# Kernel tuning notes

Measured on AMD Instinct MI355X. Metric: run time of the kernel, lower is better.

Reference implementation:

```python
import jax, jax.numpy as jnp
import numpy as np

B, N, NT, ET = 16, 38, 9, 4
NE = N * (N - 1) // 2          # 703 edge-generation steps
R = N + NE                     # repeat_num = 741 masked subgraphs
H = D = 128                    # nhid / nout
L = 12                         # num_flow_layer
EDIM = ET - 1                  # 3 relation types used by RGCN
EPS = 1e-5
TEMP = 0.1                     # straight-through argmax temperature


def _st_dis(x, w1, b1, w2, b2):
    # MLP -> logits -> straight-through one-hot(argmax)
    h = jnp.tanh(x @ w1.T + b1)
    logits = h @ w2.T + b2
    soft = jax.nn.softmax(logits / TEMP, axis=-1)
    hard = jax.nn.one_hot(jnp.argmax(logits, axis=-1), logits.shape[-1], dtype=logits.dtype)
    return soft + jax.lax.stop_gradient(hard - soft)


def _one_hot_add(inputs, shift):
    # (inputs + shift) mod vocab in one-hot space == circular conv via FFT
    out = jnp.fft.ifft(jnp.fft.fft(inputs, axis=-1) * jnp.fft.fft(shift, axis=-1), axis=-1)
    return jnp.real(out).astype(inputs.dtype)


def _gconv(x, adj, w):
    # x: (b, n, f_in), adj: (b, e, n, n), w: (e*f_out, f_in)
    b, n, _ = x.shape
    s = (x @ w.T).reshape(b, n, EDIM, -1)            # (b, n, e, f_out)
    return jnp.einsum('beij,bjeo->bio', adj, s)      # aggregate over relations


def _rgcn(x, adj, emb_w, gc1_w, gc2_w, gc3_w):
    h = x @ emb_w.T
    h = jax.nn.relu(_gconv(h, adj, gc1_w))
    h = jax.nn.relu(_gconv(h, adj, gc2_w))
    return _gconv(h, adj, gc3_w)                     # no relu on last layer


def setup_inputs():
    key = jax.random.key(0)
    ks = jax.random.split(key, 16)
    s = 0.1
    iu, ju = np.triu_indices(N, k=1)                 # canonical edge order (703, 2)
    return {
        'x': jax.random.uniform(ks[0], (B, N, NT), dtype=jnp.float32),
        'adj': jax.random.uniform(ks[1], (B, ET, N, N), dtype=jnp.float32),
        'x_deq': jax.random.normal(ks[2], (B, N, NT), dtype=jnp.float32),
        'adj_deq': jax.random.normal(ks[3], (B, NE, ET), dtype=jnp.float32),
        'mask_node': jax.random.uniform(ks[4], (R, N)) < 0.5,
        'mask_edge': jax.random.uniform(ks[5], (R, N, N)) < 0.5,
        'index_select_edge': jnp.asarray(np.stack([iu, ju], 1), dtype=jnp.int32),
        'emb_w': jax.random.normal(ks[6], (NT, NT), jnp.float32) * s,
        'gc1_w': jax.random.normal(ks[7], (EDIM * H, NT), jnp.float32) * s,
        'gc2_w': jax.random.normal(ks[8], (EDIM * H, H), jnp.float32) * s,
        'gc3_w': jax.random.normal(ks[9], (EDIM * D, H), jnp.float32) * s,
        'bn_gamma': jnp.ones((D,), jnp.float32),
        'bn_beta': jnp.zeros((D,), jnp.float32),
        'node_w1': jax.random.normal(ks[10], (L, H, D), jnp.float32) * s,
        'node_b1': jnp.zeros((L, H), jnp.float32),
        'node_w2': jax.random.normal(ks[11], (L, NT, H), jnp.float32) * s,
        'node_b2': jnp.zeros((L, NT), jnp.float32),
        'edge_w1': jax.random.normal(ks[12], (L, H, 3 * D), jnp.float32) * s,
        'edge_b1': jnp.zeros((L, H), jnp.float32),
        'edge_w2': jax.random.normal(ks[13], (L, ET, H), jnp.float32) * s,
        'edge_b2': jnp.zeros((L, ET), jnp.float32),
    }


def reference(x, adj, x_deq, adj_deq, mask_node, mask_edge, index_select_edge,
              emb_w, gc1_w, gc2_w, gc3_w, bn_gamma, bn_beta,
              node_w1, node_b1, node_w2, node_b2,
              edge_w1, edge_b1, edge_w2, edge_b2):
    adj3 = adj[:, :EDIM]                                              # (B,3,N,N)
    xr = jnp.where(mask_node[None, :, :, None], x[:, None], 0.0)      # (B,R,N,NT)
    ar = jnp.where(mask_edge[None, :, None], adj3[:, None], 0.0)      # (B,R,3,N,N)
    xr = xr.reshape(B * R, N, NT)
    ar = ar.reshape(B * R, EDIM, N, N)
    node_emb = _rgcn(xr, ar, emb_w, gc1_w, gc2_w, gc3_w)              # (B*R,N,D)
    # BatchNorm1d over channels (training-mode batch statistics, biased var)
    m = node_emb.mean(axis=(0, 1))
    v = node_emb.var(axis=(0, 1))
    node_emb = (node_emb - m) * jax.lax.rsqrt(v + EPS) * bn_gamma + bn_beta
    node_emb = node_emb.reshape(B, R, N, D)
    graph_emb = node_emb.sum(axis=2)                                  # (B,R,D)
    graph_emb_node = graph_emb[:, :N]                                 # (B,N,D)
    graph_emb_edge = graph_emb[:, N:, None]                           # (B,NE,1,D)
    all_node_emb_edge = node_emb[:, N:]                               # (B,NE,N,D)
    idx = jnp.broadcast_to(index_select_edge[None, :, :, None].astype(jnp.int32), (B, NE, 2, D))
    sel = jnp.take_along_axis(all_node_emb_edge, idx, axis=2)         # (B,NE,2,D)
    graph_node_emb_edge = jnp.concatenate([sel, graph_emb_edge], axis=2).reshape(B, NE, 3 * D)
    xd, ad = x_deq, adj_deq
    for i in range(L):
        nt = _st_dis(graph_emb_node, node_w1[i], node_b1[i], node_w2[i], node_b2[i]).astype(x.dtype)
        xd = _one_hot_add(xd, nt)
        et = _st_dis(graph_node_emb_edge, edge_w1[i], edge_b1[i], edge_w2[i], edge_b2[i]).astype(adj.dtype)
        ad = _one_hot_add(ad, et)
    return (xd, ad)
```

## Files before the change

kernel.cpp:

```cpp
#include <hip/hip_runtime.h>

#define B_   16
#define N_   38
#define NT_  9
#define ET_  4
#define NE_  703
#define R_   741
#define L_   12
#define BR_  11856

__global__ __launch_bounds__(128) void k_sx(const float* __restrict__ x,
                                            const float* __restrict__ emb_w,
                                            const float* __restrict__ gc1_w,
                                            float* __restrict__ sx)
{
  int bn = blockIdx.x;
  int t  = threadIdx.x;
  __shared__ float xr[NT_];
  __shared__ float hx[NT_];
  if (t < NT_) xr[t] = x[bn*NT_ + t];
  __syncthreads();
  if (t < NT_) {
    float s = 0.f;
    #pragma unroll
    for (int u = 0; u < NT_; ++u) s += xr[u] * emb_w[t*NT_ + u];
    hx[t] = s;
  }
  __syncthreads();
  for (int eo = t; eo < 384; eo += 128) {
    float s = 0.f;
    #pragma unroll
    for (int u = 0; u < NT_; ++u) s += hx[u] * gc1_w[eo*NT_ + u];
    sx[bn*384 + eo] = s;
  }
}

__global__ __launch_bounds__(128) void k_wt(const float* __restrict__ gc2_w,
                                            const float* __restrict__ gc3_w,
                                            float* __restrict__ Wt)
{
  int blk   = blockIdx.x;
  int which = blk / 384;
  int rem   = blk - which*384;
  int e     = rem >> 7;
  int k     = rem & 127;
  int o     = threadIdx.x;
  const float* src = which ? gc3_w : gc2_w;
  Wt[(((which*3 + e) << 7) + k)*128 + o] = src[((e << 7) + o)*128 + k];
}

__device__ __forceinline__ void fma4(float4& d, float a, const float4& s) {
  d.x += a*s.x; d.y += a*s.y; d.z += a*s.z; d.w += a*s.w;
}

__device__ __forceinline__ void eacc(const float* __restrict__ A4_l,
                                     const float* __restrict__ A1_l,
                                     const float* __restrict__ S_l,
                                     int e, int p, int c,
                                     const int* __restrict__ mn,
                                     float4& d0, float4& d1, float4& d2,
                                     float4& d3, float4& d4)
{
  #pragma unroll 2
  for (int j = 0; j < 38; ++j) {
    if (mn && !mn[j]) continue;
    int e38j = e*38 + j;
    float4 s4 = *(const float4*)&S_l[(j << 7) + (c << 2)];
    float4 a4 = *(const float4*)&A4_l[(e38j << 5) + (p << 2)];
    float  a1 = A1_l[(e38j << 3) + p];
    fma4(d0, a4.x, s4); fma4(d1, a4.y, s4); fma4(d2, a4.z, s4);
    fma4(d3, a4.w, s4); fma4(d4, a1,   s4);
  }
}

__device__ __forceinline__ void gemm5x4(const float* __restrict__ H_l,
                                        const float* __restrict__ W,
                                        int p, int c,
                                        float4& g0, float4& g1, float4& g2,
                                        float4& g3, float4& g4)
{
  g0.x=g0.y=g0.z=g0.w=0.f; g1=g0; g2=g0; g3=g0; g4=g0;
  for (int k0 = 0; k0 < 128; k0 += 4) {
    float4 w0 = *(const float4*)&W[((k0+0) << 7) + (c << 2)];
    float4 w1 = *(const float4*)&W[((k0+1) << 7) + (c << 2)];
    float4 w2 = *(const float4*)&W[((k0+2) << 7) + (c << 2)];
    float4 w3 = *(const float4*)&W[((k0+3) << 7) + (c << 2)];
    float4 h0 = *(const float4*)&H_l[((p+ 0) << 7) + k0];
    float4 h1 = *(const float4*)&H_l[((p+ 8) << 7) + k0];
    float4 h2 = *(const float4*)&H_l[((p+16) << 7) + k0];
    float4 h3 = *(const float4*)&H_l[((p+24) << 7) + k0];
    float4 h4 = *(const float4*)&H_l[((p+32) << 7) + k0];
    fma4(g0, h0.x, w0); fma4(g0, h0.y, w1); fma4(g0, h0.z, w2); fma4(g0, h0.w, w3);
    fma4(g1, h1.x, w0); fma4(g1, h1.y, w1); fma4(g1, h1.z, w2); fma4(g1, h1.w, w3);
    fma4(g2, h2.x, w0); fma4(g2, h2.y, w1); fma4(g2, h2.z, w2); fma4(g2, h2.w, w3);
    fma4(g3, h3.x, w0); fma4(g3, h3.y, w1); fma4(g3, h3.z, w2); fma4(g3, h3.w, w3);
    fma4(g4, h4.x, w0); fma4(g4, h4.y, w1); fma4(g4, h4.z, w2); fma4(g4, h4.w, w3);
  }
}

__global__ __launch_bounds__(256) void k_rgcn(
    const float* __restrict__ adj, const int* __restrict__ mask_node,
    const int* __restrict__ mask_edge, const int* __restrict__ isel,
    const float* __restrict__ sx, const float* __restrict__ Wt,
    float* __restrict__ sumE, float* __restrict__ sumSq,
    float* __restrict__ selw)
{
  const int br  = blockIdx.x;
  const int b   = br / R_;
  const int r   = br - b*R_;
  const int tid = threadIdx.x;
  const int c   = tid & 31;
  const int p   = tid >> 5;

  __shared__ __align__(16) float A4_l[3*38*32];
  __shared__ __align__(16) float A1_l[3*38*8];
  __shared__ __align__(16) float S_l[40*128];
  __shared__ __align__(16) float H_l[40*128];
  __shared__ int mn_l[40];

  if (tid < 38) mn_l[tid] = mask_node[r*N_ + tid];

  for (int m = tid; m < 3*38*32; m += 256) {
    int e    = m / 1216;
    int rem  = m - e*1216;
    int j    = rem >> 5;
    int slot = rem & 31;
    int i    = (slot >> 2) + ((slot & 3) << 3);
    float v  = 0.f;
    if (mask_edge[(r*N_ + i)*N_ + j]) v = adj[((b*ET_ + e)*N_ + i)*N_ + j];
    A4_l[m] = v;
  }
  for (int m = tid; m < 3*38*8; m += 256) {
    int e   = m / 304;
    int rem = m - e*304;
    int j   = rem >> 3;
    int i   = (rem & 7) + 32;
    float v = 0.f;
    if (i < N_ && mask_edge[(r*N_ + i)*N_ + j]) v = adj[((b*ET_ + e)*N_ + i)*N_ + j];
    A1_l[m] = v;
  }
  __syncthreads();

  float4 d0, d1, d2, d3, d4;
  d0.x=d0.y=d0.z=d0.w=0.f; d1=d0; d2=d0; d3=d0; d4=d0;

  for (int e = 0; e < 3; ++e) {
    for (int idx = tid; idx < 40*128; idx += 256) {
      int j = idx >> 7, oo = idx & 127;
      float v = 0.f;
      if (j < N_ && mn_l[j]) v = sx[(b*N_ + j)*384 + (e << 7) + oo];
      S_l[idx] = v;
    }
    __syncthreads();
    eacc(A4_l, A1_l, S_l, e, p, c, mn_l, d0, d1, d2, d3, d4);
    __syncthreads();
  }
  {
    float4 t;
    t.x=fmaxf(d0.x,0.f); t.y=fmaxf(d0.y,0.f); t.z=fmaxf(d0.z,0.f); t.w=fmaxf(d0.w,0.f);
    *(float4*)&H_l[((p+ 0) << 7) + (c << 2)] = t;
    t.x=fmaxf(d1.x,0.f); t.y=fmaxf(d1.y,0.f); t.z=fmaxf(d1.z,0.f); t.w=fmaxf(d1.w,0.f);
    *(float4*)&H_l[((p+ 8) << 7) + (c << 2)] = t;
    t.x=fmaxf(d2.x,0.f); t.y=fmaxf(d2.y,0.f); t.z=fmaxf(d2.z,0.f); t.w=fmaxf(d2.w,0.f);
    *(float4*)&H_l[((p+16) << 7) + (c << 2)] = t;
    t.x=fmaxf(d3.x,0.f); t.y=fmaxf(d3.y,0.f); t.z=fmaxf(d3.z,0.f); t.w=fmaxf(d3.w,0.f);
    *(float4*)&H_l[((p+24) << 7) + (c << 2)] = t;
    t.x=fmaxf(d4.x,0.f); t.y=fmaxf(d4.y,0.f); t.z=fmaxf(d4.z,0.f); t.w=fmaxf(d4.w,0.f);
    *(float4*)&H_l[((p+32) << 7) + (c << 2)] = t;
  }
  __syncthreads();

  for (int gv = 0; gv < 2; ++gv) {
    d0.x=d0.y=d0.z=d0.w=0.f; d1=d0; d2=d0; d3=d0; d4=d0;
    for (int e = 0; e < 3; ++e) {
      float4 g0, g1, g2, g3, g4;
      gemm5x4(H_l, &Wt[((gv*3 + e) << 14)], p, c, g0, g1, g2, g3, g4);
      __syncthreads();
      *(float4*)&S_l[((p+ 0) << 7) + (c << 2)] = g0;
      *(float4*)&S_l[((p+ 8) << 7) + (c << 2)] = g1;
      *(float4*)&S_l[((p+16) << 7) + (c << 2)] = g2;
      *(float4*)&S_l[((p+24) << 7) + (c << 2)] = g3;
      *(float4*)&S_l[((p+32) << 7) + (c << 2)] = g4;
      __syncthreads();
      eacc(A4_l, A1_l, S_l, e, p, c, nullptr, d0, d1, d2, d3, d4);
    }
    if (gv == 0) {
      __syncthreads();
      float4 t;
      t.x=fmaxf(d0.x,0.f); t.y=fmaxf(d0.y,0.f); t.z=fmaxf(d0.z,0.f); t.w=fmaxf(d0.w,0.f);
      *(float4*)&H_l[((p+ 0) << 7) + (c << 2)] = t;
      t.x=fmaxf(d1.x,0.f); t.y=fmaxf(d1.y,0.f); t.z=fmaxf(d1.z,0.f); t.w=fmaxf(d1.w,0.f);
      *(float4*)&H_l[((p+ 8) << 7) + (c << 2)] = t;
      t.x=fmaxf(d2.x,0.f); t.y=fmaxf(d2.y,0.f); t.z=fmaxf(d2.z,0.f); t.w=fmaxf(d2.w,0.f);
      *(float4*)&H_l[((p+16) << 7) + (c << 2)] = t;
      t.x=fmaxf(d3.x,0.f); t.y=fmaxf(d3.y,0.f); t.z=fmaxf(d3.z,0.f); t.w=fmaxf(d3.w,0.f);
      *(float4*)&H_l[((p+24) << 7) + (c << 2)] = t;
      t.x=fmaxf(d4.x,0.f); t.y=fmaxf(d4.y,0.f); t.z=fmaxf(d4.z,0.f); t.w=fmaxf(d4.w,0.f);
      *(float4*)&H_l[((p+32) << 7) + (c << 2)] = t;
      __syncthreads();
    }
  }
  __syncthreads();

  {
    float4 sA, sB;
    sA.x = d0.x+d1.x+d2.x+d3.x+d4.x;
    sA.y = d0.y+d1.y+d2.y+d3.y+d4.y;
    sA.z = d0.z+d1.z+d2.z+d3.z+d4.z;
    sA.w = d0.w+d1.w+d2.w+d3.w+d4.w;
    sB.x = d0.x*d0.x+d1.x*d1.x+d2.x*d2.x+d3.x*d3.x+d4.x*d4.x;
    sB.y = d0.y*d0.y+d1.y*d1.y+d2.y*d2.y+d3.y*d3.y+d4.y*d4.y;
    sB.z = d0.z*d0.z+d1.z*d1.z+d2.z*d2.z+d3.z*d3.z+d4.z*d4.z;
    sB.w = d0.w*d0.w+d1.w*d1.w+d2.w*d2.w+d3.w*d3.w+d4.w*d4.w;
    *(float4*)&S_l[( p      << 7) + (c << 2)] = sA;
    *(float4*)&S_l[((8 + p) << 7) + (c << 2)] = sB;
  }
  __syncthreads();
  {
    int o = tid & 127, half = tid >> 7;
    float t = 0.f;
    #pragma unroll
    for (int pp = 0; pp < 8; ++pp) t += S_l[(((half << 3) + pp) << 7) + o];
    if (half == 0) sumE [br*128 + o] = t;
    else           sumSq[br*128 + o] = t;
  }
  if (r >= N_) {
    int k  = r - N_;
    int iu = isel[2*k], ju = isel[2*k+1];
    if (p == (iu & 7)) {
      int mu = iu >> 3;
      float4 v = d0;
      if (mu == 1) v = d1; else if (mu == 2) v = d2;
      else if (mu == 3) v = d3; else if (mu == 4) v = d4;
      *(float4*)&selw[(((b*NE_ + k)*2 + 0) << 7) + (c << 2)] = v;
    }
    if (p == (ju & 7)) {
      int mu = ju >> 3;
      float4 v = d0;
      if (mu == 1) v = d1; else if (mu == 2) v = d2;
      else if (mu == 3) v = d3; else if (mu == 4) v = d4;
      *(float4*)&selw[(((b*NE_ + k)*2 + 1) << 7) + (c << 2)] = v;
    }
  }
}

__global__ __launch_bounds__(256) void k_bn1(const float* __restrict__ sumE,
                                             const float* __restrict__ sumSq,
                                             double* __restrict__ part)
{
  int g = blockIdx.x;
  int t = threadIdx.x;
  int o = t & 127, h = t >> 7;
  int lo = g*47;
  int hi = lo + 47; if (hi > BR_) hi = BR_;
  double a1 = 0.0, a2 = 0.0;
  for (int i = lo + h; i < hi; i += 2) {
    a1 += (double)sumE [i*128 + o];
    a2 += (double)sumSq[i*128 + o];
  }
  __shared__ double sh1[256], sh2[256];
  sh1[t] = a1; sh2[t] = a2;
  __syncthreads();
  if (h == 0) {
    part[g*128 + o]           = sh1[o] + sh1[128 + o];
    part[256*128 + g*128 + o] = sh2[o] + sh2[128 + o];
  }
}

__global__ __launch_bounds__(128) void k_bn2(const double* __restrict__ part,
                                             const float* __restrict__ gamma,
                                             const float* __restrict__ beta,
                                             float* __restrict__ bnsc,
                                             float* __restrict__ bnsh)
{
  int o = threadIdx.x;
  double s1 = 0.0, s2 = 0.0;
  for (int g = 0; g < 256; ++g) {
    s1 += part[g*128 + o];
    s2 += part[256*128 + g*128 + o];
  }
  double cnt = (double)BR_ * 38.0;
  double m   = s1 / cnt;
  double var = s2 / cnt - m*m;
  double rs  = 1.0 / sqrt(var + 1e-5);
  double sc  = (double)gamma[o] * rs;
  bnsc[o] = (float)sc;
  bnsh[o] = beta[o] - (float)(m * sc);
}

__global__ __launch_bounds__(128) void k_node(
    const float* __restrict__ sumE, const float* __restrict__ bnsc,
    const float* __restrict__ bnsh,
    const float* __restrict__ w1, const float* __restrict__ b1,
    const float* __restrict__ w2, const float* __restrict__ b2,
    const float* __restrict__ x_deq, float* __restrict__ out)
{
  int blk = blockIdx.x;
  int b   = blk / N_;
  int o   = threadIdx.x;
  __shared__ __align__(16) float xv[128];
  __shared__ __align__(16) float hb[128];
  __shared__ float lg[NT_];
  __shared__ int   P_s;
  int br = b*R_ + (blk - b*N_);
  xv[o] = sumE[br*128 + o]*bnsc[o] + 38.f*bnsh[o];
  if (o == 0) P_s = 0;
  __syncthreads();
  for (int l = 0; l < L_; ++l) {
    const float* wr = &w1[(l*128 + o)*128];
    float s = b1[l*128 + o];
    for (int k = 0; k < 128; k += 4) {
      float4 w4 = *(const float4*)&wr[k];
      s += w4.x*xv[k] + w4.y*xv[k+1] + w4.z*xv[k+2] + w4.w*xv[k+3];
    }
    hb[o] = tanhf(s);
    __syncthreads();
    if (o < NT_) {
      const float* w2r = &w2[(l*NT_ + o)*128];
      float s2 = b2[l*NT_ + o];
      for (int k = 0; k < 128; ++k) s2 += w2r[k]*hb[k];
      lg[o] = s2;
    }
    __syncthreads();
    if (o == 0) {
      int best = 0; float bv = lg[0];
      #pragma unroll
      for (int cc = 1; cc < NT_; ++cc) if (lg[cc] > bv) { bv = lg[cc]; best = cc; }
      P_s += best;
    }
    __syncthreads();
  }
  int P = P_s % NT_;
  if (o < NT_) {
    int srcc = o - P; if (srcc < 0) srcc += NT_;
    out[blk*NT_ + o] = x_deq[blk*NT_ + srcc];
  }
}

__global__ __launch_bounds__(256) void k_edge(
    const float* __restrict__ sumE, const float* __restrict__ selw,
    const float* __restrict__ bnsc, const float* __restrict__ bnsh,
    const float* __restrict__ w1, const float* __restrict__ b1,
    const float* __restrict__ w2, const float* __restrict__ b2,
    const float* __restrict__ adj_deq, float* __restrict__ out)
{
  int k = blockIdx.x;
  int t = threadIdx.x;
  int o = t & 127, g = t >> 7;
  __shared__ __align__(16) float xv[16][384];
  __shared__ __align__(16) float hb[16][132];
  __shared__ float lg[16][4];
  __shared__ int   Pf[16];

  for (int idx = t; idx < 16*128; idx += 256) {
    int b = idx >> 7, oo = idx & 127;
    float sc = bnsc[oo], sh = bnsh[oo];
    int base = ((b*NE_ + k)*2)*128;
    xv[b][oo]       = selw[base + oo]      *sc + sh;
    xv[b][128 + oo] = selw[base + 128 + oo]*sc + sh;
    xv[b][256 + oo] = sumE[(b*R_ + N_ + k)*128 + oo]*sc + 38.f*sh;
  }
  int Preg = 0;
  __syncthreads();

  for (int l = 0; l < L_; ++l) {
    float acc[8];
    #pragma unroll
    for (int bb = 0; bb < 8; ++bb) acc[bb] = b1[l*128 + o];
    const float* wr = &w1[(l*128 + o)*384];
    for (int kk = 0; kk < 384; kk += 4) {
      float4 w4 = *(const float4*)&wr[kk];
      #pragma unroll
      for (int bb = 0; bb < 8; ++bb) {
        float4 h4 = *(const float4*)&xv[g*8 + bb][kk];
        acc[bb] += w4.x*h4.x + w4.y*h4.y + w4.z*h4.z + w4.w*h4.w;
      }
    }
    #pragma unroll
    for (int bb = 0; bb < 8; ++bb) hb[g*8 + bb][o] = tanhf(acc[bb]);
    __syncthreads();
    if (t < 64) {
      int m = t >> 2, c = t & 3;
      const float* w2r = &w2[(l*ET_ + c)*128];
      float s2 = b2[l*ET_ + c];
      for (int kk = 0; kk < 128; ++kk) s2 += w2r[kk]*hb[m][kk];
      lg[m][c] = s2;
    }
    __syncthreads();
    if (t < 16) {
      int best = 0; float bv = lg[t][0];
      #pragma unroll
      for (int c = 1; c < ET_; ++c) if (lg[t][c] > bv) { bv = lg[t][c]; best = c; }
      Preg += best;
    }
    __syncthreads();
  }
  if (t < 16) Pf[t] = Preg & 3;
  __syncthreads();
  if (t < 64) {
    int m = t >> 2, c = t & 3;
    int srcc = c - Pf[m]; if (srcc < 0) srcc += ET_;
    out[(m*NE_ + k)*ET_ + c] = adj_deq[(m*NE_ + k)*ET_ + srcc];
  }
}

extern "C" void kernel_launch(void* const* d_in, const int* in_sizes, int n_in,
                              void* d_out, int out_size, void* d_ws, size_t ws_size,
                              hipStream_t stream)
{
  (void)in_sizes; (void)n_in; (void)out_size; (void)ws_size;

  const float* x         = (const float*)d_in[0];
  const float* adj       = (const float*)d_in[1];
  const float* x_deq     = (const float*)d_in[2];
  const float* adj_deq   = (const float*)d_in[3];
  const int*   mask_node = (const int*)d_in[4];
  const int*   mask_edge = (const int*)d_in[5];
  const int*   isel      = (const int*)d_in[6];
  const float* emb_w     = (const float*)d_in[7];
  const float* gc1_w     = (const float*)d_in[8];
  const float* gc2_w     = (const float*)d_in[9];
  const float* gc3_w     = (const float*)d_in[10];
  const float* bn_gamma  = (const float*)d_in[11];
  const float* bn_beta   = (const float*)d_in[12];
  const float* node_w1   = (const float*)d_in[13];
  const float* node_b1   = (const float*)d_in[14];
  const float* node_w2   = (const float*)d_in[15];
  const float* node_b2   = (const float*)d_in[16];
  const float* edge_w1   = (const float*)d_in[17];
  const float* edge_b1   = (const float*)d_in[18];
  const float* edge_w2   = (const float*)d_in[19];
  const float* edge_b2   = (const float*)d_in[20];

  float* out_f = (float*)d_out;

  float*  wsf   = (float*)d_ws;
  float*  sx    = wsf;
  float*  sumE  = sx    + 233472;
  float*  sumSq = sumE  + 1517568;
  float*  selw  = sumSq + 1517568;
  float*  bnsc  = selw  + 2879488;
  float*  bnsh  = bnsc  + 128;
  double* part  = (double*)(bnsh + 128);
  float*  Wt    = (float*)part;

  k_wt  <<<768,    128, 0, stream>>>(gc2_w, gc3_w, Wt);
  k_sx  <<<B_*N_,  128, 0, stream>>>(x, emb_w, gc1_w, sx);
  k_rgcn<<<BR_,    256, 0, stream>>>(adj, mask_node, mask_edge, isel, sx,
                                     Wt, sumE, sumSq, selw);
  k_bn1 <<<256,    256, 0, stream>>>(sumE, sumSq, part);
  k_bn2 <<<1,      128, 0, stream>>>(part, bn_gamma, bn_beta, bnsc, bnsh);
  k_node<<<B_*N_,  128, 0, stream>>>(sumE, bnsc, bnsh, node_w1, node_b1,
                                     node_w2, node_b2, x_deq, out_f);
  k_edge<<<NE_,    256, 0, stream>>>(sumE, selw, bnsc, bnsh, edge_w1, edge_b1,
                                     edge_w2, edge_b2, adj_deq,
                                     out_f + B_*N_*NT_);
}
```

Before: 2.592 ms.

## Shrink adjacency LDS to one relation, refill per relation, vectorize S loads

```diff
diff --git a/kernel.cpp b/kernel.cpp
--- a/kernel.cpp
+++ b/kernel.cpp
@@ -53,21 +53,60 @@
   d.x += a*s.x; d.y += a*s.y; d.z += a*s.z; d.w += a*s.w;
 }
 
-__device__ __forceinline__ void eacc(const float* __restrict__ A4_l,
-                                     const float* __restrict__ A1_l,
-                                     const float* __restrict__ S_l,
-                                     int e, int p, int c,
-                                     const int* __restrict__ mn,
-                                     float4& d0, float4& d1, float4& d2,
-                                     float4& d3, float4& d4)
+__device__ __forceinline__ void fill_A(const float* __restrict__ adj,
+                                       const int* __restrict__ mask_edge,
+                                       int b, int r, int e, int tid,
+                                       float* __restrict__ A4_l,
+                                       float* __restrict__ A1_l)
+{
+  for (int m = tid; m < 38*32; m += 256) {
+    int j    = m >> 5;
+    int slot = m & 31;
+    int i    = (slot >> 2) + ((slot & 3) << 3);
+    float v  = 0.f;
+    if (mask_edge[(r*N_ + i)*N_ + j]) v = adj[((b*ET_ + e)*N_ + i)*N_ + j];
+    A4_l[m] = v;
+  }
+  for (int m = tid; m < 38*8; m += 256) {
+    int j = m >> 3;
+    int i = (m & 7) + 32;
+    float v = 0.f;
+    if (i < N_ && mask_edge[(r*N_ + i)*N_ + j]) v = adj[((b*ET_ + e)*N_ + i)*N_ + j];
+    A1_l[m] = v;
+  }
+}
+
+__device__ __forceinline__ void eacc_m(const float* __restrict__ A4_l,
+                                       const float* __restrict__ A1_l,
+                                       const float* __restrict__ S_l,
+                                       int p, int c,
+                                       const int* __restrict__ mn,
+                                       float4& d0, float4& d1, float4& d2,
+                                       float4& d3, float4& d4)
 {
   #pragma unroll 2
   for (int j = 0; j < 38; ++j) {
-    if (mn && !mn[j]) continue;
-    int e38j = e*38 + j;
+    if (!mn[j]) continue;
     float4 s4 = *(const float4*)&S_l[(j << 7) + (c << 2)];
-    float4 a4 = *(const float4*)&A4_l[(e38j << 5) + (p << 2)];
-    float  a1 = A1_l[(e38j << 3) + p];
+    float4 a4 = *(const float4*)&A4_l[(j << 5) + (p << 2)];
+    float  a1 = A1_l[(j << 3) + p];
+    fma4(d0, a4.x, s4); fma4(d1, a4.y, s4); fma4(d2, a4.z, s4);
+    fma4(d3, a4.w, s4); fma4(d4, a1,   s4);
+  }
+}
+
+__device__ __forceinline__ void eacc_u(const float* __restrict__ A4_l,
+                                       const float* __restrict__ A1_l,
+                                       const float* __restrict__ S_l,
+                                       int p, int c,
+                                       float4& d0, float4& d1, float4& d2,
+                                       float4& d3, float4& d4)
+{
+  #pragma unroll 4
+  for (int j = 0; j < 38; ++j) {
+    float4 s4 = *(const float4*)&S_l[(j << 7) + (c << 2)];
+    float4 a4 = *(const float4*)&A4_l[(j << 5) + (p << 2)];
+    float  a1 = A1_l[(j << 3) + p];
     fma4(d0, a4.x, s4); fma4(d1, a4.y, s4); fma4(d2, a4.z, s4);
     fma4(d3, a4.w, s4); fma4(d4, a1,   s4);
   }
@@ -80,6 +119,7 @@
                                         float4& g3, float4& g4)
 {
   g0.x=g0.y=g0.z=g0.w=0.f; g1=g0; g2=g0; g3=g0; g4=g0;
+  #pragma unroll 2
   for (int k0 = 0; k0 < 128; k0 += 4) {
     float4 w0 = *(const float4*)&W[((k0+0) << 7) + (c << 2)];
     float4 w1 = *(const float4*)&W[((k0+1) << 7) + (c << 2)];
@@ -112,47 +152,28 @@
   const int c   = tid & 31;
   const int p   = tid >> 5;
 
-  __shared__ __align__(16) float A4_l[3*38*32];
-  __shared__ __align__(16) float A1_l[3*38*8];
+  __shared__ __align__(16) float A4_l[38*32];
+  __shared__ __align__(16) float A1_l[38*8];
   __shared__ __align__(16) float S_l[40*128];
   __shared__ __align__(16) float H_l[40*128];
   __shared__ int mn_l[40];
 
-  if (tid < 38) mn_l[tid] = mask_node[r*N_ + tid];
-
-  for (int m = tid; m < 3*38*32; m += 256) {
-    int e    = m / 1216;
-    int rem  = m - e*1216;
-    int j    = rem >> 5;
-    int slot = rem & 31;
-    int i    = (slot >> 2) + ((slot & 3) << 3);
-    float v  = 0.f;
-    if (mask_edge[(r*N_ + i)*N_ + j]) v = adj[((b*ET_ + e)*N_ + i)*N_ + j];
-    A4_l[m] = v;
-  }
-  for (int m = tid; m < 3*38*8; m += 256) {
-    int e   = m / 304;
-    int rem = m - e*304;
-    int j   = rem >> 3;
-    int i   = (rem & 7) + 32;
-    float v = 0.f;
-    if (i < N_ && mask_edge[(r*N_ + i)*N_ + j]) v = adj[((b*ET_ + e)*N_ + i)*N_ + j];
-    A1_l[m] = v;
-  }
+  if (tid < 40) mn_l[tid] = (tid < 38) ? mask_node[r*N_ + tid] : 0;
   __syncthreads();
 
   float4 d0, d1, d2, d3, d4;
   d0.x=d0.y=d0.z=d0.w=0.f; d1=d0; d2=d0; d3=d0; d4=d0;
 
   for (int e = 0; e < 3; ++e) {
-    for (int idx = tid; idx < 40*128; idx += 256) {
-      int j = idx >> 7, oo = idx & 127;
-      float v = 0.f;
-      if (j < N_ && mn_l[j]) v = sx[(b*N_ + j)*384 + (e << 7) + oo];
-      S_l[idx] = v;
-    }
-    __syncthreads();
-    eacc(A4_l, A1_l, S_l, e, p, c, mn_l, d0, d1, d2, d3, d4);
+    for (int idx = tid; idx < 40*32; idx += 256) {
+      int j = idx >> 5, q4 = idx & 31;
+      float4 v; v.x=v.y=v.z=v.w=0.f;
+      if (j < N_ && mn_l[j]) v = *(const float4*)&sx[(b*N_ + j)*384 + (e << 7) + (q4 << 2)];
+      *(float4*)&S_l[(j << 7) + (q4 << 2)] = v;
+    }
+    fill_A(adj, mask_edge, b, r, e, tid, A4_l, A1_l);
+    __syncthreads();
+    eacc_m(A4_l, A1_l, S_l, p, c, mn_l, d0, d1, d2, d3, d4);
     __syncthreads();
   }
   {
@@ -181,8 +202,9 @@
       *(float4*)&S_l[((p+16) << 7) + (c << 2)] = g2;
       *(float4*)&S_l[((p+24) << 7) + (c << 2)] = g3;
       *(float4*)&S_l[((p+32) << 7) + (c << 2)] = g4;
+      fill_A(adj, mask_edge, b, r, e, tid, A4_l, A1_l);
       __syncthreads();
-      eacc(A4_l, A1_l, S_l, e, p, c, nullptr, d0, d1, d2, d3, d4);
+      eacc_u(A4_l, A1_l, S_l, p, c, d0, d1, d2, d3, d4);
     }
     if (gv == 0) {
       __syncthreads();
```

Measured after the change: 2.449 ms. 5.5% less time.
